# Optimization experiments

Hardware: AMD Instinct MI355X
Metric: run time of the kernel (lower is better)

## Reference

```python
import jax, jax.numpy as jnp
import numpy as np

B, T, D, H = 4, 2048, 1024, 16
DH = D // H


def setup_inputs() -> dict:
    key = jax.random.key(0)
    ks = jax.random.split(key, 11)
    s = 1.0 / np.sqrt(D)
    return {
        "q": jax.random.normal(ks[0], (B, T, D), jnp.float32),
        "k": jax.random.normal(ks[1], (B, T, D), jnp.float32),
        "v": jax.random.normal(ks[2], (B, T, D), jnp.float32),
        "Wq": jax.random.normal(ks[3], (D, D), jnp.float32) * s,
        "bq": jax.random.normal(ks[4], (D,), jnp.float32) * s,
        "Wk": jax.random.normal(ks[5], (D, D), jnp.float32) * s,
        "bk": jax.random.normal(ks[6], (D,), jnp.float32) * s,
        "Wv": jax.random.normal(ks[7], (D, D), jnp.float32) * s,
        "bv": jax.random.normal(ks[8], (D,), jnp.float32) * s,
        "Wo": jax.random.normal(ks[9], (D, D), jnp.float32) * s,
        "bo": jax.random.normal(ks[10], (D,), jnp.float32) * s,
    }


def _heads(x):
    # (B, T, D) -> (B, H, T, DH)
    return x.reshape(B, T, H, DH).transpose(0, 2, 1, 3)


def reference(q, k, v, Wq, bq, Wk, bk, Wv, bv, Wo, bo):
    qh = _heads(q @ Wq + bq)
    kh = _heads(k @ Wk + bk)
    vh = _heads(v @ Wv + bv)
    scale = 1.0 / np.sqrt(DH).astype(np.float32)
    # full (B, H, T, T) score matrix, as in the original module
    scores = jnp.einsum("bhqd,bhkd->bhqk", qh, kh) * scale
    causal = jnp.tril(jnp.ones((T, T), dtype=bool))  # keep j <= i (causal intent)
    scores = jnp.where(causal, scores, -jnp.inf)
    attn = jax.nn.softmax(scores, axis=-1)
    ctx = jnp.einsum("bhqk,bhkd->bhqd", attn, vh)
    ctx = ctx.transpose(0, 2, 1, 3).reshape(B, T, D)
    return ctx @ Wo + bo
```

## Files before the change

kernel.cpp:

```cpp
#include <hip/hip_runtime.h>
#include <hip/hip_bf16.h>

#define NB 4
#define NT 2048
#define ND 1024
#define NH 16
#define NDH 64
#define NM (NB*NT)

typedef __bf16 bf16_t;
typedef bf16_t bf16x4 __attribute__((ext_vector_type(4)));
typedef bf16_t bf16x8 __attribute__((ext_vector_type(8)));
typedef float f32x2 __attribute__((ext_vector_type(2)));
typedef float f32x4 __attribute__((ext_vector_type(4)));
typedef unsigned int u32x4 __attribute__((ext_vector_type(4)));

__device__ __forceinline__ void gload_lds16(const bf16_t* g, bf16_t* l) {
  __builtin_amdgcn_global_load_lds(
      (const __attribute__((address_space(1))) unsigned int*)g,
      (__attribute__((address_space(3))) unsigned int*)l, 16, 0, 0);
}

__device__ __forceinline__ float exp2_hw(float x) {
  float r;
  asm("v_exp_f32 %0, %1" : "=v"(r) : "v"(x));
  return r;
}

#define CVTPK(lo, hi) ({ unsigned r_; \
  asm("v_cvt_pk_bf16_f32 %0, %1, %2" : "=v"(r_) : "v"(lo), "v"(hi)); r_; })

__global__ void transpose_cvt4(const float* __restrict__ w0, const float* __restrict__ w1,
                               const float* __restrict__ w2, const float* __restrict__ w3,
                               bf16_t* __restrict__ o0, bf16_t* __restrict__ o1,
                               bf16_t* __restrict__ o2, bf16_t* __restrict__ o3) {
  __shared__ float tile[32][33];
  const float* in = blockIdx.z == 0 ? w0 : blockIdx.z == 1 ? w1 : blockIdx.z == 2 ? w2 : w3;
  bf16_t* out     = blockIdx.z == 0 ? o0 : blockIdx.z == 1 ? o1 : blockIdx.z == 2 ? o2 : o3;
  int n0 = blockIdx.x * 32, k0 = blockIdx.y * 32;
  int tx = threadIdx.x & 31, ty = threadIdx.x >> 5;
  #pragma unroll
  for (int r = ty; r < 32; r += 8)
    tile[r][tx] = in[(size_t)(k0 + r) * ND + n0 + tx];
  __syncthreads();
  #pragma unroll
  for (int r = ty; r < 32; r += 8)
    out[(size_t)(n0 + r) * ND + k0 + tx] = (bf16_t)tile[tx][r];
}

__global__ void cvt3(const float* __restrict__ q, const float* __restrict__ k,
                     const float* __restrict__ v, bf16_t* __restrict__ oq,
                     bf16_t* __restrict__ ok, bf16_t* __restrict__ ov) {
  const float* in = blockIdx.y == 0 ? q : blockIdx.y == 1 ? k : v;
  bf16_t* out     = blockIdx.y == 0 ? oq : blockIdx.y == 1 ? ok : ov;
  int i = blockIdx.x * 256 + threadIdx.x;
  float4 vv = ((const float4*)in)[i];
  bf16x4 o;
  o[0] = (bf16_t)vv.x; o[1] = (bf16_t)vv.y; o[2] = (bf16_t)vv.z; o[3] = (bf16_t)vv.w;
  ((bf16x4*)out)[i] = o;
}

#define GEMM8_CORE(Aptr, Btptr)                                                     \
  const int K = ND;                                                                 \
  const int tid = threadIdx.x, lane = tid & 63, wid = tid >> 6;                     \
  const int wm = wid >> 2, wn = wid & 3;                                            \
  const int lrow = lane & 15, lg = lane >> 4, rb = lg << 2;                         \
  const int tm = blockIdx.y * 128, tn = blockIdx.x * 256;                           \
  const int d0 = tid * 16, d1 = 8192 + tid * 16;                                    \
  const int r0s = d0 >> 7, r1s = d1 >> 7;                                           \
  const int cb0 = (d0 & 127) ^ ((r0s & 7) << 4);                                    \
  const int cb1 = (d1 & 127) ^ ((r1s & 7) << 4);                                    \
  const int e0 = d0 >> 1, e1 = d1 >> 1;                                             \
  const bf16_t* aC0 = (Aptr) + (size_t)(tm + r0s) * K + (cb0 >> 1);                 \
  const bf16_t* aC1 = (Aptr) + (size_t)(tm + r1s) * K + (cb1 >> 1);                 \
  const bf16_t* b0C0 = (Btptr) + (size_t)(tn + r0s) * K + (cb0 >> 1);               \
  const bf16_t* b0C1 = (Btptr) + (size_t)(tn + r1s) * K + (cb1 >> 1);               \
  const bf16_t* b1C0 = b0C0 + (size_t)128 * K;                                      \
  const bf16_t* b1C1 = b0C1 + (size_t)128 * K;                                      \
  const int swzk = (lrow & 7) << 4;                                                 \
  const int kc0 = (lg * 16) ^ swzk;                                                 \
  const int kc1 = (64 + lg * 16) ^ swzk;                                            \
  const int aBase = wm * 8192 + lrow * 128;                                         \
  const int bBase = (wn & 1) * 8192 + lrow * 128;                                   \
  f32x4 acc[4][4];                                                                  \
  _Pragma("unroll")                                                                 \
  for (int m = 0; m < 4; ++m)                                                       \
    _Pragma("unroll")                                                               \
    for (int n = 0; n < 4; ++n) {                                                   \
      f32x4 zz = {0.f, 0.f, 0.f, 0.f};                                              \
      acc[m][n] = zz;                                                               \
    }                                                                               \
  gload_lds16(aC0,  &S[0][0][0] + e0); gload_lds16(aC1,  &S[0][0][0] + e1);         \
  gload_lds16(b0C0, &S[0][1][0] + e0); gload_lds16(b0C1, &S[0][1][0] + e1);         \
  gload_lds16(b1C0, &S[0][2][0] + e0); gload_lds16(b1C1, &S[0][2][0] + e1);         \
  gload_lds16(b0C0 + 64, &S[1][1][0] + e0); gload_lds16(b0C1 + 64, &S[1][1][0] + e1);\
  gload_lds16(b1C0 + 64, &S[1][2][0] + e0); gload_lds16(b1C1 + 64, &S[1][2][0] + e1);\
  asm volatile("s_waitcnt vmcnt(4)\n\ts_barrier" ::: "memory");                     \
  const int NS = K / 64;                                                            \
  _Pragma("unroll 1")                                                               \
  for (int s = 0; s < NS; ++s) {                                                    \
    const int b = s & 1;                                                            \
    const char* aReg = (const char*)&S[b][0][0];                                    \
    const char* bReg = (const char*)&S[b][1 + (wn >> 1)][0];                        \
    bf16x8 bfr[4][2];                                                               \
    _Pragma("unroll")                                                               \
    for (int n = 0; n < 4; ++n) {                                                   \
      bfr[n][0] = *(const bf16x8*)(bReg + n * 2048 + bBase + kc0);                  \
      bfr[n][1] = *(const bf16x8*)(bReg + n * 2048 + bBase + kc1);                  \
    }                                                                               \
    bf16x8 afrA[2][2];                                                              \
    afrA[0][0] = *(const bf16x8*)(aReg + 0 * 2048 + aBase + kc0);                   \
    afrA[0][1] = *(const bf16x8*)(aReg + 0 * 2048 + aBase + kc1);                   \
    afrA[1][0] = *(const bf16x8*)(aReg + 1 * 2048 + aBase + kc0);                   \
    afrA[1][1] = *(const bf16x8*)(aReg + 1 * 2048 + aBase + kc1);                   \
    if (s + 1 < NS) {                                                               \
      gload_lds16(aC0 + (s + 1) * 64, &S[b ^ 1][0][0] + e0);                        \
      gload_lds16(aC1 + (s + 1) * 64, &S[b ^ 1][0][0] + e1);                        \
    }                                                                               \
    asm volatile("s_barrier" ::: "memory");                                         \
    __builtin_amdgcn_s_setprio(1);                                                  \
    _Pragma("unroll")                                                               \
    for (int mm = 0; mm < 2; ++mm)                                                  \
      _Pragma("unroll")                                                             \
      for (int n = 0; n < 4; ++n)                                                   \
        _Pragma("unroll")                                                           \
        for (int kk = 0; kk < 2; ++kk)                                              \
          acc[mm][n] = __builtin_amdgcn_mfma_f32_16x16x32_bf16(                     \
              afrA[mm][kk], bfr[n][kk], acc[mm][n], 0, 0, 0);                       \
    __builtin_amdgcn_s_setprio(0);                                                  \
    asm volatile("s_waitcnt lgkmcnt(0)\n\ts_barrier" ::: "memory");                 \
    bf16x8 afrB[2][2];                                                              \
    afrB[0][0] = *(const bf16x8*)(aReg + 2 * 2048 + aBase + kc0);                   \
    afrB[0][1] = *(const bf16x8*)(aReg + 2 * 2048 + aBase + kc1);                   \
    afrB[1][0] = *(const bf16x8*)(aReg + 3 * 2048 + aBase + kc0);                   \
    afrB[1][1] = *(const bf16x8*)(aReg + 3 * 2048 + aBase + kc1);                   \
    if (s + 2 < NS) {                                                               \
      gload_lds16(b0C0 + (s + 2) * 64, &S[b][1][0] + e0);                           \
      gload_lds16(b0C1 + (s + 2) * 64, &S[b][1][0] + e1);                           \
      gload_lds16(b1C0 + (s + 2) * 64, &S[b][2][0] + e0);                           \
      gload_lds16(b1C1 + (s + 2) * 64, &S[b][2][0] + e1);                           \
    }                                                                               \
    asm volatile("s_barrier" ::: "memory");                                         \
    __builtin_amdgcn_s_setprio(1);                                                  \
    _Pragma("unroll")                                                               \
    for (int mm = 0; mm < 2; ++mm)                                                  \
      _Pragma("unroll")                                                             \
      for (int n = 0; n < 4; ++n)                                                   \
        _Pragma("unroll")                                                           \
        for (int kk = 0; kk < 2; ++kk)                                              \
          acc[2 + mm][n] = __builtin_amdgcn_mfma_f32_16x16x32_bf16(                 \
              afrB[mm][kk], bfr[n][kk], acc[2 + mm][n], 0, 0, 0);                   \
    __builtin_amdgcn_s_setprio(0);                                                  \
    if (s < NS - 2)                                                                 \
      asm volatile("s_waitcnt vmcnt(4) lgkmcnt(0)\n\ts_barrier" ::: "memory");      \
    else if (s == NS - 2)                                                           \
      asm volatile("s_waitcnt vmcnt(0) lgkmcnt(0)\n\ts_barrier" ::: "memory");      \
    else                                                                            \
      asm volatile("s_waitcnt lgkmcnt(0)" ::: "memory");                            \
  }

__global__ __launch_bounds__(512, 2) void gemm8_qkv(
    const bf16_t* __restrict__ Aq, const bf16_t* __restrict__ Ak, const bf16_t* __restrict__ Av,
    const bf16_t* __restrict__ Bq, const bf16_t* __restrict__ Bk, const bf16_t* __restrict__ Bv,
    const float* __restrict__ bq, const float* __restrict__ bk, const float* __restrict__ bv,
    bf16_t* __restrict__ Qh, bf16_t* __restrict__ Kh, bf16_t* __restrict__ Vt,
    float qscale) {
  __shared__ bf16_t S[2][3][8192];
  const int z = blockIdx.z;
  const bf16_t* A    = z == 0 ? Aq : z == 1 ? Ak : Av;
  const bf16_t* Bt   = z == 0 ? Bq : z == 1 ? Bk : Bv;
  const float*  bias = z == 0 ? bq : z == 1 ? bk : bv;
  const float   scale = z == 0 ? qscale : 1.0f;
  bf16_t* outp = z == 0 ? Qh : z == 1 ? Kh : Vt;

  GEMM8_CORE(A, Bt)

  #pragma unroll
  for (int n = 0; n < 4; ++n) {
    const int ncol = tn + wn * 64 + n * 16 + lrow;
    const float bv = bias[ncol];
    const int h = ncol >> 6, dh = ncol & (NDH - 1);
    #pragma unroll
    for (int m = 0; m < 4; ++m) {
      const int m0 = tm + wm * 64 + m * 16 + rb;
      const int bb = m0 >> 11, t0 = m0 & (NT - 1);
      if (z == 2) {
        bf16x4 o;
        #pragma unroll
        for (int r = 0; r < 4; ++r) o[r] = (bf16_t)(acc[m][n][r] + bv);
        size_t idx = ((size_t)(bb * NH + h) * NDH + dh) * NT + t0;
        *(bf16x4*)(outp + idx) = o;
      } else {
        #pragma unroll
        for (int r = 0; r < 4; ++r) {
          float val = (acc[m][n][r] + bv) * scale;
          size_t idx = ((size_t)(bb * NH + h) * NT + t0 + r) * NDH + dh;
          outp[idx] = (bf16_t)val;
        }
      }
    }
  }
}

__global__ __launch_bounds__(512, 2) void gemm8_out(
    const bf16_t* __restrict__ A, const bf16_t* __restrict__ Bt,
    const float* __restrict__ bias, float* __restrict__ outp) {
  __shared__ bf16_t S[2][3][8192];

  GEMM8_CORE(A, Bt)

  #pragma unroll
  for (int n = 0; n < 4; ++n) {
    const int ncol = tn + wn * 64 + n * 16 + lrow;
    const float bv = bias[ncol];
    #pragma unroll
    for (int m = 0; m < 4; ++m) {
      const int m0 = tm + wm * 64 + m * 16 + rb;
      #pragma unroll
      for (int r = 0; r < 4; ++r)
        outp[(size_t)(m0 + r) * ND + ncol] = acc[m][n][r] + bv;
    }
  }
}

__device__ __forceinline__ bf16x8 lds_swz_read(const bf16_t* base, int row, int colb) {
  return *(const bf16x8*)((const char*)base + row * 128 + (colb ^ ((row & 7) << 4)));
}

__global__ __launch_bounds__(256) void attn_kernel(
    const bf16_t* __restrict__ Qh, const bf16_t* __restrict__ Kh,
    const bf16_t* __restrict__ Vt, bf16_t* __restrict__ ctx) {
  __shared__ bf16_t Ks[2][64 * 64];
  __shared__ bf16_t Vs[2][64 * 64];
  const int tid  = threadIdx.x;
  const int lane = tid & 63;
  const int wid  = tid >> 6;

  const int work    = (blockIdx.x & 7) * 128 + (blockIdx.x >> 3);
  const int bh      = work >> 4;
  const int pairIdx = work & 15;
  const int b = bh >> 4, h = bh & 15;

  const bf16_t* Qbh = Qh + (size_t)bh * NT * NDH;
  const bf16_t* Kbh = Kh + (size_t)bh * NT * NDH;
  const bf16_t* Vbh = Vt + (size_t)bh * NDH * NT;

  const int lrow = lane & 15;
  const int lg   = lane >> 4;

  bf16x8 ones;
  #pragma unroll
  for (int i = 0; i < 8; ++i) ones[i] = (bf16_t)1.0f;

  const char *kS0, *kS1, *vS0, *vS1;
  {
    int o0 = wid * 1024 + lane * 16;
    int o1 = 4096 + wid * 1024 + lane * 16;
    int r0_ = o0 >> 7, r1_ = o1 >> 7;
    kS0 = (const char*)Kbh + (o0 ^ ((r0_ & 7) << 4));
    kS1 = (const char*)Kbh + (o1 ^ ((r1_ & 7) << 4));
    int c0 = (o0 & 127) ^ ((r0_ & 7) << 4);
    int c1 = (o1 & 127) ^ ((r1_ & 7) << 4);
    vS0 = (const char*)Vbh + (size_t)r0_ * (NT * 2) + c0;
    vS1 = (const char*)Vbh + (size_t)r1_ * (NT * 2) + c1;
  }
  const int ldsOff = wid * 512;

  auto stage = [&](int t, int buf) {
    bf16_t* kb = Ks[buf];
    bf16_t* vb = Vs[buf];
    size_t kOff = (size_t)t * 8192;
    size_t vOff = (size_t)t * 128;
    gload_lds16((const bf16_t*)(kS0 + kOff), kb + ldsOff);
    gload_lds16((const bf16_t*)(kS1 + kOff), kb + 2048 + ldsOff);
    gload_lds16((const bf16_t*)(vS0 + vOff), vb + ldsOff);
    gload_lds16((const bf16_t*)(vS1 + vOff), vb + 2048 + ldsOff);
  };

  #pragma unroll 1
  for (int half = 0; half < 2; ++half) {
    const int qidx = half ? (31 - pairIdx) : pairIdx;
    const int r0   = qidx * 64 + wid * 16;
    const int qg   = r0 + lrow;

    bf16x8 qf0 = *(const bf16x8*)&Qbh[(size_t)(r0 + lrow) * NDH + lg * 8];
    bf16x8 qf1 = *(const bf16x8*)&Qbh[(size_t)(r0 + lrow) * NDH + 32 + lg * 8];

    f32x4 acc[4], accS;
    #pragma unroll
    for (int d = 0; d < 4; ++d) { f32x4 z = {0.f, 0.f, 0.f, 0.f}; acc[d] = z; }
    { f32x4 z = {0.f, 0.f, 0.f, 0.f}; accS = z; }

    __syncthreads();
    stage(0, 0);
    int cur = 0;

    #pragma unroll 1
    for (int t = 0; t <= qidx; ++t) {
      asm volatile("s_waitcnt vmcnt(0)\n\ts_barrier" ::: "memory");
      if (t < qidx) stage(t + 1, cur ^ 1);

      const bf16_t* ksCur = Ks[cur];
      const bf16_t* vsCur = Vs[cur];

      f32x4 sg[4];
      #pragma unroll
      for (int g = 0; g < 4; ++g) { f32x4 z = {0.f, 0.f, 0.f, 0.f}; sg[g] = z; }
      __builtin_amdgcn_s_setprio(1);
      #pragma unroll
      for (int g = 0; g < 4; ++g) {
        bf16x8 kfa = lds_swz_read(ksCur, g * 16 + lrow, lg * 16);
        sg[g] = __builtin_amdgcn_mfma_f32_16x16x32_bf16(kfa, qf0, sg[g], 0, 0, 0);
        bf16x8 kfb = lds_swz_read(ksCur, g * 16 + lrow, 64 + lg * 16);
        sg[g] = __builtin_amdgcn_mfma_f32_16x16x32_bf16(kfb, qf1, sg[g], 0, 0, 0);
      }
      __builtin_amdgcn_s_setprio(0);

      if (t == qidx) {
        const int jb = t * 64;
        #pragma unroll
        for (int g = 0; g < 4; ++g)
          #pragma unroll
          for (int r = 0; r < 4; ++r)
            if (jb + g * 16 + lg * 4 + r > qg) sg[g][r] = -1e30f;
      }

      #pragma unroll
      for (int g = 0; g < 4; ++g)
        #pragma unroll
        for (int r = 0; r < 4; ++r) sg[g][r] = exp2_hw(sg[g][r]);

      unsigned W00 = CVTPK(sg[0][0], sg[0][1]), W01 = CVTPK(sg[0][2], sg[0][3]);
      unsigned W10 = CVTPK(sg[1][0], sg[1][1]), W11 = CVTPK(sg[1][2], sg[1][3]);
      unsigned W20 = CVTPK(sg[2][0], sg[2][1]), W21 = CVTPK(sg[2][2], sg[2][3]);
      unsigned W30 = CVTPK(sg[3][0], sg[3][1]), W31 = CVTPK(sg[3][2], sg[3][3]);
      unsigned w00, w01, w02, w03, w10, w11, w12, w13;
      { unsigned a = W00, bb = W10;
        asm("v_permlane32_swap_b32 %0, %1" : "+v"(a), "+v"(bb));
        asm("v_permlane16_swap_b32 %0, %1" : "+v"(a), "+v"(bb));
        w00 = a; w02 = bb; }
      { unsigned a = W01, bb = W11;
        asm("v_permlane32_swap_b32 %0, %1" : "+v"(a), "+v"(bb));
        asm("v_permlane16_swap_b32 %0, %1" : "+v"(a), "+v"(bb));
        w01 = a; w03 = bb; }
      { unsigned a = W20, bb = W30;
        asm("v_permlane32_swap_b32 %0, %1" : "+v"(a), "+v"(bb));
        asm("v_permlane16_swap_b32 %0, %1" : "+v"(a), "+v"(bb));
        w10 = a; w12 = bb; }
      { unsigned a = W21, bb = W31;
        asm("v_permlane32_swap_b32 %0, %1" : "+v"(a), "+v"(bb));
        asm("v_permlane16_swap_b32 %0, %1" : "+v"(a), "+v"(bb));
        w11 = a; w13 = bb; }
      u32x4 c0 = {w00, w01, w02, w03};
      u32x4 c1 = {w10, w11, w12, w13};
      bf16x8 pf0 = __builtin_bit_cast(bf16x8, c0);
      bf16x8 pf1 = __builtin_bit_cast(bf16x8, c1);

      __builtin_amdgcn_s_setprio(1);
      accS = __builtin_amdgcn_mfma_f32_16x16x32_bf16(ones, pf0, accS, 0, 0, 0);
      #pragma unroll
      for (int d = 0; d < 4; ++d) {
        bf16x8 vf0 = lds_swz_read(vsCur, d * 16 + lrow, lg * 16);
        acc[d] = __builtin_amdgcn_mfma_f32_16x16x32_bf16(vf0, pf0, acc[d], 0, 0, 0);
        bf16x8 vf1 = lds_swz_read(vsCur, d * 16 + lrow, 64 + lg * 16);
        acc[d] = __builtin_amdgcn_mfma_f32_16x16x32_bf16(vf1, pf1, acc[d], 0, 0, 0);
      }
      accS = __builtin_amdgcn_mfma_f32_16x16x32_bf16(ones, pf1, accS, 0, 0, 0);
      __builtin_amdgcn_s_setprio(0);

      cur ^= 1;
    }

    float inv = 1.f / accS[0];
    f32x4 inv4 = {inv, inv, inv, inv};
    size_t orow = ((size_t)b * NT + qg) * ND + h * NDH;
    #pragma unroll
    for (int d2 = 0; d2 < 4; ++d2) {
      f32x4 vv = acc[d2] * inv4;
      bf16x4 o;
      #pragma unroll
      for (int r = 0; r < 4; ++r) o[r] = (bf16_t)vv[r];
      *(bf16x4*)&ctx[orow + d2 * 16 + lg * 4] = o;
    }
  }
}

extern "C" void kernel_launch(void* const* d_in, const int* in_sizes, int n_in,
                              void* d_out, int out_size, void* d_ws, size_t ws_size,
                              hipStream_t stream) {
  const float* q  = (const float*)d_in[0];
  const float* k  = (const float*)d_in[1];
  const float* v  = (const float*)d_in[2];
  const float* Wq = (const float*)d_in[3];
  const float* bq = (const float*)d_in[4];
  const float* Wk = (const float*)d_in[5];
  const float* bk = (const float*)d_in[6];
  const float* Wv = (const float*)d_in[7];
  const float* bv = (const float*)d_in[8];
  const float* Wo = (const float*)d_in[9];
  const float* bo = (const float*)d_in[10];
  float* out = (float*)d_out;

  char* ws = (char*)d_ws;
  const size_t szMK = (size_t)NM * ND * sizeof(bf16_t);
  const size_t szW  = (size_t)ND * ND * sizeof(bf16_t);
  bf16_t* Xq  = (bf16_t*)d_out;
  bf16_t* Xk  = Xq + (size_t)NM * ND;
  bf16_t* Xv  = (bf16_t*)(ws);
  bf16_t* ctx = (bf16_t*)(ws);
  bf16_t* Qh  = (bf16_t*)(ws + szMK);
  bf16_t* Kh  = (bf16_t*)(ws + 2 * szMK);
  bf16_t* Vt  = (bf16_t*)(ws + 3 * szMK);
  bf16_t* Wqt = (bf16_t*)(ws + 4 * szMK);
  bf16_t* Wkt = (bf16_t*)(ws + 4 * szMK + szW);
  bf16_t* Wvt = (bf16_t*)(ws + 4 * szMK + 2 * szW);
  bf16_t* Wot = (bf16_t*)(ws + 4 * szMK + 3 * szW);

  dim3 tb(256);
  transpose_cvt4<<<dim3(ND / 32, ND / 32, 4), tb, 0, stream>>>(Wq, Wk, Wv, Wo,
                                                               Wqt, Wkt, Wvt, Wot);

  const float qscale = 0.125f * 1.44269504f;

  cvt3<<<dim3(NM * ND / 4 / 256, 3), tb, 0, stream>>>(q, k, v, Xq, Xk, Xv);

  gemm8_qkv<<<dim3(ND / 256, NM / 128, 3), dim3(512), 0, stream>>>(
      Xq, Xk, Xv, Wqt, Wkt, Wvt, bq, bk, bv, Qh, Kh, Vt, qscale);

  attn_kernel<<<dim3(NB * NH * 16), tb, 0, stream>>>(Qh, Kh, Vt, ctx);

  gemm8_out<<<dim3(ND / 256, NM / 128), dim3(512), 0, stream>>>(ctx, Wot, bo, out);
}
```

Before: 181.7 us.

## Shrink GEMM block tile to 128x128 with four waves per block

```diff
diff --git a/kernel.cpp b/kernel.cpp
--- a/kernel.cpp
+++ b/kernel.cpp
@@ -63,25 +63,30 @@
 #define GEMM8_CORE(Aptr, Btptr)                                                     \
   const int K = ND;                                                                 \
   const int tid = threadIdx.x, lane = tid & 63, wid = tid >> 6;                     \
-  const int wm = wid >> 2, wn = wid & 3;                                            \
+  const int wm = wid >> 1, wn = wid & 1;                                            \
   const int lrow = lane & 15, lg = lane >> 4, rb = lg << 2;                         \
-  const int tm = blockIdx.y * 128, tn = blockIdx.x * 256;                           \
-  const int d0 = tid * 16, d1 = 8192 + tid * 16;                                    \
-  const int r0s = d0 >> 7, r1s = d1 >> 7;                                           \
+  const int tm = blockIdx.y * 128, tn = blockIdx.x * 128;                           \
+  const int d0 = tid * 16, d1 = 4096 + tid * 16,                                    \
+            d2 = 8192 + tid * 16, d3 = 12288 + tid * 16;                            \
+  const int r0s = d0 >> 7, r1s = d1 >> 7, r2s = d2 >> 7, r3s = d3 >> 7;             \
   const int cb0 = (d0 & 127) ^ ((r0s & 7) << 4);                                    \
   const int cb1 = (d1 & 127) ^ ((r1s & 7) << 4);                                    \
-  const int e0 = d0 >> 1, e1 = d1 >> 1;                                             \
+  const int cb2 = (d2 & 127) ^ ((r2s & 7) << 4);                                    \
+  const int cb3 = (d3 & 127) ^ ((r3s & 7) << 4);                                    \
+  const int e0 = d0 >> 1, e1 = d1 >> 1, e2 = d2 >> 1, e3 = d3 >> 1;                 \
   const bf16_t* aC0 = (Aptr) + (size_t)(tm + r0s) * K + (cb0 >> 1);                 \
   const bf16_t* aC1 = (Aptr) + (size_t)(tm + r1s) * K + (cb1 >> 1);                 \
-  const bf16_t* b0C0 = (Btptr) + (size_t)(tn + r0s) * K + (cb0 >> 1);               \
-  const bf16_t* b0C1 = (Btptr) + (size_t)(tn + r1s) * K + (cb1 >> 1);               \
-  const bf16_t* b1C0 = b0C0 + (size_t)128 * K;                                      \
-  const bf16_t* b1C1 = b0C1 + (size_t)128 * K;                                      \
+  const bf16_t* aC2 = (Aptr) + (size_t)(tm + r2s) * K + (cb2 >> 1);                 \
+  const bf16_t* aC3 = (Aptr) + (size_t)(tm + r3s) * K + (cb3 >> 1);                 \
+  const bf16_t* bC0 = (Btptr) + (size_t)(tn + r0s) * K + (cb0 >> 1);                \
+  const bf16_t* bC1 = (Btptr) + (size_t)(tn + r1s) * K + (cb1 >> 1);                \
+  const bf16_t* bC2 = (Btptr) + (size_t)(tn + r2s) * K + (cb2 >> 1);                \
+  const bf16_t* bC3 = (Btptr) + (size_t)(tn + r3s) * K + (cb3 >> 1);                \
   const int swzk = (lrow & 7) << 4;                                                 \
   const int kc0 = (lg * 16) ^ swzk;                                                 \
   const int kc1 = (64 + lg * 16) ^ swzk;                                            \
   const int aBase = wm * 8192 + lrow * 128;                                         \
-  const int bBase = (wn & 1) * 8192 + lrow * 128;                                   \
+  const int bBase = wn * 8192 + lrow * 128;                                         \
   f32x4 acc[4][4];                                                                  \
   _Pragma("unroll")                                                                 \
   for (int m = 0; m < 4; ++m)                                                       \
@@ -90,18 +95,19 @@
       f32x4 zz = {0.f, 0.f, 0.f, 0.f};                                              \
       acc[m][n] = zz;                                                               \
     }                                                                               \
-  gload_lds16(aC0,  &S[0][0][0] + e0); gload_lds16(aC1,  &S[0][0][0] + e1);         \
-  gload_lds16(b0C0, &S[0][1][0] + e0); gload_lds16(b0C1, &S[0][1][0] + e1);         \
-  gload_lds16(b1C0, &S[0][2][0] + e0); gload_lds16(b1C1, &S[0][2][0] + e1);         \
-  gload_lds16(b0C0 + 64, &S[1][1][0] + e0); gload_lds16(b0C1 + 64, &S[1][1][0] + e1);\
-  gload_lds16(b1C0 + 64, &S[1][2][0] + e0); gload_lds16(b1C1 + 64, &S[1][2][0] + e1);\
+  gload_lds16(aC0, &S[0][0][0] + e0); gload_lds16(aC1, &S[0][0][0] + e1);           \
+  gload_lds16(aC2, &S[0][0][0] + e2); gload_lds16(aC3, &S[0][0][0] + e3);           \
+  gload_lds16(bC0, &S[0][1][0] + e0); gload_lds16(bC1, &S[0][1][0] + e1);           \
+  gload_lds16(bC2, &S[0][1][0] + e2); gload_lds16(bC3, &S[0][1][0] + e3);           \
+  gload_lds16(bC0 + 64, &S[1][1][0] + e0); gload_lds16(bC1 + 64, &S[1][1][0] + e1); \
+  gload_lds16(bC2 + 64, &S[1][1][0] + e2); gload_lds16(bC3 + 64, &S[1][1][0] + e3); \
   asm volatile("s_waitcnt vmcnt(4)\n\ts_barrier" ::: "memory");                     \
   const int NS = K / 64;                                                            \
   _Pragma("unroll 1")                                                               \
   for (int s = 0; s < NS; ++s) {                                                    \
     const int b = s & 1;                                                            \
     const char* aReg = (const char*)&S[b][0][0];                                    \
-    const char* bReg = (const char*)&S[b][1 + (wn >> 1)][0];                        \
+    const char* bReg = (const char*)&S[b][1][0];                                    \
     bf16x8 bfr[4][2];                                                               \
     _Pragma("unroll")                                                               \
     for (int n = 0; n < 4; ++n) {                                                   \
@@ -116,6 +122,8 @@
     if (s + 1 < NS) {                                                               \
       gload_lds16(aC0 + (s + 1) * 64, &S[b ^ 1][0][0] + e0);                        \
       gload_lds16(aC1 + (s + 1) * 64, &S[b ^ 1][0][0] + e1);                        \
+      gload_lds16(aC2 + (s + 1) * 64, &S[b ^ 1][0][0] + e2);                        \
+      gload_lds16(aC3 + (s + 1) * 64, &S[b ^ 1][0][0] + e3);                        \
     }                                                                               \
     asm volatile("s_barrier" ::: "memory");                                         \
     __builtin_amdgcn_s_setprio(1);                                                  \
@@ -135,10 +143,10 @@
     afrB[1][0] = *(const bf16x8*)(aReg + 3 * 2048 + aBase + kc0);                   \
     afrB[1][1] = *(const bf16x8*)(aReg + 3 * 2048 + aBase + kc1);                   \
     if (s + 2 < NS) {                                                               \
-      gload_lds16(b0C0 + (s + 2) * 64, &S[b][1][0] + e0);                           \
-      gload_lds16(b0C1 + (s + 2) * 64, &S[b][1][0] + e1);                           \
-      gload_lds16(b1C0 + (s + 2) * 64, &S[b][2][0] + e0);                           \
-      gload_lds16(b1C1 + (s + 2) * 64, &S[b][2][0] + e1);                           \
+      gload_lds16(bC0 + (s + 2) * 64, &S[b][1][0] + e0);                            \
+      gload_lds16(bC1 + (s + 2) * 64, &S[b][1][0] + e1);                            \
+      gload_lds16(bC2 + (s + 2) * 64, &S[b][1][0] + e2);                            \
+      gload_lds16(bC3 + (s + 2) * 64, &S[b][1][0] + e3);                            \
     }                                                                               \
     asm volatile("s_barrier" ::: "memory");                                         \
     __builtin_amdgcn_s_setprio(1);                                                  \
@@ -159,13 +167,13 @@
       asm volatile("s_waitcnt lgkmcnt(0)" ::: "memory");                            \
   }
 
-__global__ __launch_bounds__(512, 2) void gemm8_qkv(
+__global__ __launch_bounds__(256, 2) void gemm8_qkv(
     const bf16_t* __restrict__ Aq, const bf16_t* __restrict__ Ak, const bf16_t* __restrict__ Av,
     const bf16_t* __restrict__ Bq, const bf16_t* __restrict__ Bk, const bf16_t* __restrict__ Bv,
     const float* __restrict__ bq, const float* __restrict__ bk, const float* __restrict__ bv,
     bf16_t* __restrict__ Qh, bf16_t* __restrict__ Kh, bf16_t* __restrict__ Vt,
     float qscale) {
-  __shared__ bf16_t S[2][3][8192];
+  __shared__ bf16_t S[2][2][8192];
   const int z = blockIdx.z;
   const bf16_t* A    = z == 0 ? Aq : z == 1 ? Ak : Av;
   const bf16_t* Bt   = z == 0 ? Bq : z == 1 ? Bk : Bv;
@@ -202,10 +210,10 @@
   }
 }
 
-__global__ __launch_bounds__(512, 2) void gemm8_out(
+__global__ __launch_bounds__(256, 2) void gemm8_out(
     const bf16_t* __restrict__ A, const bf16_t* __restrict__ Bt,
     const float* __restrict__ bias, float* __restrict__ outp) {
-  __shared__ bf16_t S[2][3][8192];
+  __shared__ bf16_t S[2][2][8192];
 
   GEMM8_CORE(A, Bt)
 
@@ -424,10 +432,10 @@
 
   cvt3<<<dim3(NM * ND / 4 / 256, 3), tb, 0, stream>>>(q, k, v, Xq, Xk, Xv);
 
-  gemm8_qkv<<<dim3(ND / 256, NM / 128, 3), dim3(512), 0, stream>>>(
+  gemm8_qkv<<<dim3(ND / 128, NM / 128, 3), tb, 0, stream>>>(
       Xq, Xk, Xv, Wqt, Wkt, Wvt, bq, bk, bv, Qh, Kh, Vt, qscale);
 
   attn_kernel<<<dim3(NB * NH * 16), tb, 0, stream>>>(Qh, Kh, Vt, ctx);
 
-  gemm8_out<<<dim3(ND / 256, NM / 128), dim3(512), 0, stream>>>(ctx, Wot, bo, out);
-}
+  gemm8_out<<<dim3(ND / 128, NM / 128), tb, 0, stream>>>(ctx, Wot, bo, out);
+}
```

After: 185.8 us. 2.3% more time.
